# Optimization experiments

Measured on AMD Instinct MI355X. Metric: run time of the kernel, lower is better.

The kernel has to match this reference:

```python
import jax, jax.numpy as jnp
import numpy as np

TOP_K = 2
E = 8      # num_experts
D = 1024   # model dim
F = 2048   # expert hidden dim = int(2*3072/3), already a multiple of 256
B, S = 2, 1024


def setup_inputs() -> dict:
    key = jax.random.key(0)
    ks = jax.random.split(key, 8)
    sc = 0.02
    return {
        "x_bsD": jax.random.normal(ks[0], (B, S, D), dtype=jnp.float32),
        "router_DE": jax.random.normal(ks[1], (D, E), dtype=jnp.float32) * sc,
        "w_in_shared_FD": jax.random.normal(ks[2], (F, D), dtype=jnp.float32) * sc,
        "w_out_shared_DF": jax.random.normal(ks[3], (D, F), dtype=jnp.float32) * sc,
        "w_swiglu_FD": jax.random.normal(ks[4], (F, D), dtype=jnp.float32) * sc,
        "w_in_eDF": jax.random.normal(ks[5], (E, D, F), dtype=jnp.float32) * sc,
        "w_swiglu_eDF": jax.random.normal(ks[6], (E, D, F), dtype=jnp.float32) * sc,
        "w_out_eFD": jax.random.normal(ks[7], (E, F, D), dtype=jnp.float32) * sc,
    }


def reference(x_bsD, router_DE, w_in_shared_FD, w_out_shared_DF, w_swiglu_FD,
              w_in_eDF, w_swiglu_eDF, w_out_eFD):
    b, s, d = x_bsD.shape
    x_aD = x_bsD.reshape(-1, d)                      # [a, D]
    a = x_aD.shape[0]

    # Router (token choice): top-k per token, others masked to -inf
    scores_aE = x_aD @ router_DE                      # [a, E]
    topv_aK, topi_aK = jax.lax.top_k(scores_aE, TOP_K)
    masked_aE = jnp.full_like(scores_aE, -jnp.inf)
    masked_aE = masked_aE.at[jnp.arange(a)[:, None], topi_aK].set(topv_aK)
    # sigmoid(-inf) == 0 -> non-selected (expert, token) pairs contribute nothing
    gates_Ea = jax.nn.sigmoid(masked_aE.astype(jnp.float32)).astype(x_aD.dtype).T  # [E, a]

    # Dispatch: router_indices_EG == arange(a) per expert, so gather == broadcast
    routed_in_EaD = x_aD[None, :, :] * gates_Ea[:, :, None]   # [E, a, D]
    routed_in_EaD = jax.lax.stop_gradient(routed_in_EaD)      # matches .detach()

    # Per-expert bmm SwiGLU
    mid_EaF = jnp.einsum('ead,edf->eaf', routed_in_EaD, w_in_eDF)
    sw_EaF = jnp.einsum('ead,edf->eaf', routed_in_EaD, w_swiglu_eDF)
    h_EaF = jax.nn.silu(mid_EaF) * sw_EaF
    out_EaD = jnp.einsum('eaf,efd->ead', h_EaF, w_out_eFD)

    # Shared expert (computed under torch.no_grad in the original)
    shared_aF = jax.nn.silu(x_aD @ w_in_shared_FD.T) * (x_aD @ w_swiglu_FD.T)
    shared_out_aD = jax.lax.stop_gradient(shared_aF @ w_out_shared_DF.T)

    # Combine: scatter_add with per-expert arange indices == sum over experts
    out_aD = shared_out_aD + jnp.sum(out_EaD, axis=0)
    return out_aD.reshape(b, s, d)
```

## Files before the change

kernel.cpp:

```cpp
#include <hip/hip_runtime.h>
#include <hip/hip_bf16.h>

#define A_TOK 2048
#define DDIM 1024
#define FDIM 2048
#define NEXP 8
#define NE9 9
#define SLOTS_R (2 * A_TOK)
#define SLOTS_T (SLOTS_R + A_TOK)

typedef __attribute__((ext_vector_type(8))) short short8v;
typedef __attribute__((ext_vector_type(4))) float f32x4;

#define BARRIER() asm volatile("s_barrier" ::: "memory")
#define VMCNT(n) asm volatile("s_waitcnt vmcnt(" #n ")" ::: "memory")

__device__ __forceinline__ void lds16(const void* g, void* l) {
  __builtin_amdgcn_global_load_lds((const __attribute__((address_space(1))) void*)g,
                                   (__attribute__((address_space(3))) void*)l, 16, 0, 0);
}

__device__ __forceinline__ float sigmoidf_(float x) { return 1.f / (1.f + __expf(-x)); }

__device__ __forceinline__ void stage_unit(const ushort* gbase, size_t grow0,
                                           int K, int k0, char* lds, int tid) {
  int o = tid * 16;
  int row = o >> 6;
  int g = (o >> 4) & 3;
  int gg = g ^ ((row >> 1) & 3);
  lds16((const char*)(gbase + (grow0 + row) * (size_t)K + k0 + gg * 8), lds + o);
}

__global__ void k_cvt3(const float* __restrict__ s0, const float* __restrict__ s1,
                       const float* __restrict__ s2, __hip_bfloat16* __restrict__ d0,
                       __hip_bfloat16* __restrict__ d1, __hip_bfloat16* __restrict__ d2) {
  const float* in = blockIdx.z == 0 ? s0 : (blockIdx.z == 1 ? s1 : s2);
  __hip_bfloat16* out = blockIdx.z == 0 ? d0 : (blockIdx.z == 1 ? d1 : d2);
  int j = (blockIdx.x * blockDim.x + threadIdx.x) * 4;
  float4 v = *(const float4*)(in + j);
  out[j + 0] = __float2bfloat16(v.x);
  out[j + 1] = __float2bfloat16(v.y);
  out[j + 2] = __float2bfloat16(v.z);
  out[j + 3] = __float2bfloat16(v.w);
}

__global__ void k_transpose(const float* __restrict__ in, __hip_bfloat16* __restrict__ out,
                            int R, int C) {
  __shared__ __hip_bfloat16 tile[64][66];
  size_t zofs = (size_t)blockIdx.z * R * C;
  in += zofs; out += zofs;
  int r0 = blockIdx.y * 64, c0 = blockIdx.x * 64;
  int rr = threadIdx.x >> 6;
  int cc = threadIdx.x & 63;
#pragma unroll
  for (int i = 0; i < 16; i++) {
    int r = i * 4 + rr;
    tile[r][cc] = __float2bfloat16(in[(size_t)(r0 + r) * C + c0 + cc]);
  }
  __syncthreads();
#pragma unroll
  for (int i = 0; i < 16; i++) {
    int c = i * 4 + rr;
    out[(size_t)(c0 + c) * R + r0 + cc] = tile[cc][c];
  }
}

__global__ void k_router(const float* __restrict__ x, const float* __restrict__ rw,
                         __hip_bfloat16* __restrict__ xbf, int* __restrict__ counts,
                         int* __restrict__ top_e, float* __restrict__ top_g) {
  int t = blockIdx.x * 4 + (threadIdx.x >> 6);
  int l = threadIdx.x & 63;
  const float* xr = x + (size_t)t * DDIM;
  float acc[NEXP];
#pragma unroll
  for (int e = 0; e < NEXP; e++) acc[e] = 0.f;
#pragma unroll
  for (int i = 0; i < 16; i++) {
    int d = i * 64 + l;
    float v = xr[d];
    xbf[(size_t)t * DDIM + d] = __float2bfloat16(v);
    const float* rr = rw + (size_t)d * NEXP;
#pragma unroll
    for (int e = 0; e < NEXP; e++) acc[e] += v * rr[e];
  }
#pragma unroll
  for (int e = 0; e < NEXP; e++) {
#pragma unroll
    for (int s = 32; s > 0; s >>= 1) acc[e] += __shfl_xor(acc[e], s);
  }
  if (l == 0) {
    float b1 = -1e30f, b2 = -1e30f;
    int i1 = 0, i2 = 0;
#pragma unroll
    for (int e = 0; e < NEXP; e++) {
      float v = acc[e];
      if (v > b1) { b2 = b1; i2 = i1; b1 = v; i1 = e; }
      else if (v > b2) { b2 = v; i2 = e; }
    }
    atomicAdd(&counts[i1], 1);
    atomicAdd(&counts[i2], 1);
    top_e[t * 2 + 0] = i1; top_e[t * 2 + 1] = i2;
    top_g[t * 2 + 0] = sigmoidf_(b1); top_g[t * 2 + 1] = sigmoidf_(b2);
  }
}

__global__ void k_scan(int* __restrict__ counts, int* __restrict__ offs,
                       int* __restrict__ cursor) {
  if (threadIdx.x == 0 && blockIdx.x == 0) {
    counts[NEXP] = A_TOK;
    int s = 0;
    for (int e = 0; e < NE9; e++) { offs[e] = s; s += counts[e]; cursor[e] = 0; }
  }
}

__global__ void k_dispatch(const float* __restrict__ x, const int* __restrict__ top_e,
                           const float* __restrict__ top_g, const int* __restrict__ offs,
                           int* __restrict__ cursor, int* __restrict__ slot_of,
                           __hip_bfloat16* __restrict__ y) {
  int t = blockIdx.x * 4 + (threadIdx.x >> 6);
  int l = threadIdx.x & 63;
  int e0 = top_e[t * 2 + 0], e1 = top_e[t * 2 + 1];
  float g0 = top_g[t * 2 + 0], g1 = top_g[t * 2 + 1];
  int s0 = 0, s1 = 0;
  if (l == 0) {
    s0 = offs[e0] + atomicAdd(&cursor[e0], 1);
    s1 = offs[e1] + atomicAdd(&cursor[e1], 1);
    slot_of[t * 2 + 0] = s0; slot_of[t * 2 + 1] = s1;
  }
  s0 = __shfl(s0, 0); s1 = __shfl(s1, 0);
  const float* xr = x + (size_t)t * DDIM;
#pragma unroll
  for (int i = 0; i < 16; i++) {
    int d = i * 64 + l;
    float v = xr[d];
    y[(size_t)s0 * DDIM + d] = __float2bfloat16(v * g0);
    y[(size_t)s1 * DDIM + d] = __float2bfloat16(v * g1);
  }
}

__global__ __launch_bounds__(512, 2) void k_mlp1(
    const ushort* __restrict__ Abase, const ushort* __restrict__ B1base,
    const ushort* __restrict__ B2base, ushort* __restrict__ Obase,
    const int* __restrict__ d_cnt, const int* __restrict__ d_off) {
  constexpr int K = DDIM, NT = DDIM / 32;
  constexpr int BUF = 40960;
  __shared__ __align__(16) char smem[3 * BUF];
  int e = blockIdx.z;
  int cnt = d_cnt[e];
  int m0 = blockIdx.y * 128;
  if (m0 >= cnt) return;
  int roff = d_off[e];
  int n0 = blockIdx.x * 256;
  const ushort* B1 = B1base + (size_t)e * FDIM * DDIM;
  const ushort* B2 = B2base + (size_t)e * FDIM * DDIM;
  int tid = threadIdx.x;
  int w = tid >> 6, l = tid & 63;
  int wm = w >> 2, wn = w & 3;
  int lr = l & 15, kg = l >> 4;
  size_t arow0 = (size_t)roff + m0;

  f32x4 acc1[4][4], acc2[4][4];
#pragma unroll
  for (int i = 0; i < 4; i++)
#pragma unroll
    for (int j = 0; j < 4; j++) {
      acc1[i][j] = {0.f, 0.f, 0.f, 0.f};
      acc2[i][j] = {0.f, 0.f, 0.f, 0.f};
    }

  auto frag = [&](const char* base, int row) -> short8v {
    return *(const short8v*)(base + row * 64 + ((kg ^ ((row >> 1) & 3)) << 4));
  };

#pragma unroll
  for (int pt = 0; pt < 2; ++pt) {
    char* bb = smem + pt * BUF;
    int k0 = pt * 32;
    stage_unit(Abase, arow0, K, k0, bb, tid);
    stage_unit(B1, (size_t)n0, K, k0, bb + 8192, tid);
    stage_unit(B1, (size_t)n0 + 128, K, k0, bb + 16384, tid);
    stage_unit(B2, (size_t)n0, K, k0, bb + 24576, tid);
    stage_unit(B2, (size_t)n0 + 128, K, k0, bb + 32768, tid);
  }
  VMCNT(5);
  BARRIER();

  char* b0 = smem;
  char* b1 = smem + BUF;
  char* b2 = smem + 2 * BUF;
  for (int t = 0; t < NT; ++t) {
    bool st = (t + 2) < NT;
    int k2 = (t + 2) * 32;
    short8v af[4], bf[4];
#pragma unroll
    for (int mf = 0; mf < 4; mf++) af[mf] = frag(b0, wm * 64 + mf * 16 + lr);
#pragma unroll
    for (int nf = 0; nf < 4; nf++) bf[nf] = frag(b0 + 8192, wn * 64 + nf * 16 + lr);
    if (st) {
      stage_unit(Abase, arow0, K, k2, b2, tid);
      stage_unit(B1, (size_t)n0, K, k2, b2 + 8192, tid);
    }
    BARRIER();
    __builtin_amdgcn_s_setprio(1);
#pragma unroll
    for (int nf = 0; nf < 4; nf++)
#pragma unroll
      for (int mf = 0; mf < 4; mf++)
        acc1[mf][nf] = __builtin_amdgcn_mfma_f32_16x16x32_bf16(af[mf], bf[nf], acc1[mf][nf], 0, 0, 0);
    __builtin_amdgcn_s_setprio(0);
    BARRIER();
#pragma unroll
    for (int nf = 0; nf < 4; nf++) bf[nf] = frag(b0 + 24576, wn * 64 + nf * 16 + lr);
    if (st) {
      stage_unit(B1, (size_t)n0 + 128, K, k2, b2 + 16384, tid);
      stage_unit(B2, (size_t)n0, K, k2, b2 + 24576, tid);
      stage_unit(B2, (size_t)n0 + 128, K, k2, b2 + 32768, tid);
    }
    BARRIER();
    __builtin_amdgcn_s_setprio(1);
#pragma unroll
    for (int nf = 0; nf < 4; nf++)
#pragma unroll
      for (int mf = 0; mf < 4; mf++)
        acc2[mf][nf] = __builtin_amdgcn_mfma_f32_16x16x32_bf16(af[mf], bf[nf], acc2[mf][nf], 0, 0, 0);
    __builtin_amdgcn_s_setprio(0);
    if (t < NT - 1) {
      if (st) { VMCNT(5); } else { VMCNT(0); }
      BARRIER();
    }
    char* tmp = b0; b0 = b1; b1 = b2; b2 = tmp;
  }

#pragma unroll
  for (int mf = 0; mf < 4; mf++)
#pragma unroll
    for (int nf = 0; nf < 4; nf++)
#pragma unroll
      for (int r = 0; r < 4; r++) {
        int row = m0 + wm * 64 + mf * 16 + kg * 4 + r;
        if (row < cnt) {
          float mid = acc1[mf][nf][r];
          float sw = acc2[mf][nf][r];
          float h = mid * sigmoidf_(mid) * sw;
          int col = n0 + wn * 64 + nf * 16 + lr;
          __hip_bfloat16 hb = __float2bfloat16(h);
          ushort u; __builtin_memcpy(&u, &hb, 2);
          Obase[((size_t)roff + row) * FDIM + col] = u;
        }
      }
}

__global__ __launch_bounds__(512, 4) void k_mlp2(
    const ushort* __restrict__ Abase, const ushort* __restrict__ Bbase,
    float* __restrict__ part, const int* __restrict__ d_cnt, const int* __restrict__ d_off) {
  constexpr int K = FDIM, NT = 1024 / 32;
  constexpr int BUF = 24576;
  __shared__ __align__(16) char smem[3 * BUF];
  int e = blockIdx.z;
  int cnt = d_cnt[e];
  int mt = blockIdx.y >> 1, kz = blockIdx.y & 1;
  int m0 = mt * 128;
  if (m0 >= cnt) return;
  int roff = d_off[e];
  int n0 = blockIdx.x * 256;
  int kbeg = kz * 1024;
  const ushort* B = Bbase + (size_t)e * DDIM * FDIM;
  int tid = threadIdx.x;
  int w = tid >> 6, l = tid & 63;
  int wm = w >> 2, wn = w & 3;
  int lr = l & 15, kg = l >> 4;
  size_t arow0 = (size_t)roff + m0;

  f32x4 acc[4][4];
#pragma unroll
  for (int i = 0; i < 4; i++)
#pragma unroll
    for (int j = 0; j < 4; j++) acc[i][j] = {0.f, 0.f, 0.f, 0.f};

  auto frag = [&](const char* base, int row) -> short8v {
    return *(const short8v*)(base + row * 64 + ((kg ^ ((row >> 1) & 3)) << 4));
  };

#pragma unroll
  for (int pt = 0; pt < 2; ++pt) {
    char* bb = smem + pt * BUF;
    int k0 = kbeg + pt * 32;
    stage_unit(Abase, arow0, K, k0, bb, tid);
    stage_unit(B, (size_t)n0, K, k0, bb + 8192, tid);
    stage_unit(B, (size_t)n0 + 128, K, k0, bb + 16384, tid);
  }
  VMCNT(3);
  BARRIER();

  char* b0 = smem;
  char* b1 = smem + BUF;
  char* b2 = smem + 2 * BUF;
  for (int t = 0; t < NT; ++t) {
    bool st = (t + 2) < NT;
    int k2 = kbeg + (t + 2) * 32;
    short8v af[4], bf[4];
#pragma unroll
    for (int mf = 0; mf < 4; mf++) af[mf] = frag(b0, wm * 64 + mf * 16 + lr);
#pragma unroll
    for (int nf = 0; nf < 4; nf++) bf[nf] = frag(b0 + 8192, wn * 64 + nf * 16 + lr);
    if (st) {
      stage_unit(Abase, arow0, K, k2, b2, tid);
      stage_unit(B, (size_t)n0, K, k2, b2 + 8192, tid);
    }
    BARRIER();
    __builtin_amdgcn_s_setprio(1);
#pragma unroll
    for (int nf = 0; nf < 2; nf++)
#pragma unroll
      for (int mf = 0; mf < 4; mf++)
        acc[mf][nf] = __builtin_amdgcn_mfma_f32_16x16x32_bf16(af[mf], bf[nf], acc[mf][nf], 0, 0, 0);
    __builtin_amdgcn_s_setprio(0);
    BARRIER();
    if (st) stage_unit(B, (size_t)n0 + 128, K, k2, b2 + 16384, tid);
    __builtin_amdgcn_s_setprio(1);
#pragma unroll
    for (int nf = 2; nf < 4; nf++)
#pragma unroll
      for (int mf = 0; mf < 4; mf++)
        acc[mf][nf] = __builtin_amdgcn_mfma_f32_16x16x32_bf16(af[mf], bf[nf], acc[mf][nf], 0, 0, 0);
    __builtin_amdgcn_s_setprio(0);
    if (t < NT - 1) {
      if (st) { VMCNT(3); } else { VMCNT(0); }
      BARRIER();
    }
    char* tmp = b0; b0 = b1; b1 = b2; b2 = tmp;
  }

  float* outp = part + (size_t)kz * SLOTS_T * DDIM;
#pragma unroll
  for (int mf = 0; mf < 4; mf++)
#pragma unroll
    for (int nf = 0; nf < 4; nf++)
#pragma unroll
      for (int r = 0; r < 4; r++) {
        int row = m0 + wm * 64 + mf * 16 + kg * 4 + r;
        if (row < cnt) {
          int col = n0 + wn * 64 + nf * 16 + lr;
          outp[((size_t)roff + row) * DDIM + col] = acc[mf][nf][r];
        }
      }
}

__global__ void k_combine(const float* __restrict__ part, const int* __restrict__ slot_of,
                          float* __restrict__ out) {
  int t = blockIdx.x;
  int d4 = threadIdx.x;
  int s0 = slot_of[t * 2 + 0], s1 = slot_of[t * 2 + 1];
  const float4* p0 = (const float4*)part;
  const float4* p1 = (const float4*)(part + (size_t)SLOTS_T * DDIM);
  size_t rq = DDIM / 4;
  float4 a = p0[(size_t)s0 * rq + d4];
  float4 b = p0[(size_t)s1 * rq + d4];
  float4 c = p0[((size_t)SLOTS_R + t) * rq + d4];
  float4 d = p1[(size_t)s0 * rq + d4];
  float4 e = p1[(size_t)s1 * rq + d4];
  float4 f = p1[((size_t)SLOTS_R + t) * rq + d4];
  float4 o;
  o.x = a.x + b.x + c.x + d.x + e.x + f.x;
  o.y = a.y + b.y + c.y + d.y + e.y + f.y;
  o.z = a.z + b.z + c.z + d.z + e.z + f.z;
  o.w = a.w + b.w + c.w + d.w + e.w + f.w;
  ((float4*)out)[(size_t)t * rq + d4] = o;
}

extern "C" void kernel_launch(void* const* d_in, const int* in_sizes, int n_in,
                              void* d_out, int out_size, void* d_ws, size_t ws_size,
                              hipStream_t stream) {
  (void)in_sizes; (void)n_in; (void)out_size; (void)ws_size;
  const float* x        = (const float*)d_in[0];
  const float* router   = (const float*)d_in[1];
  const float* w_in_sh  = (const float*)d_in[2];
  const float* w_out_sh = (const float*)d_in[3];
  const float* w_sw_sh  = (const float*)d_in[4];
  const float* w_in_e   = (const float*)d_in[5];
  const float* w_sw_e   = (const float*)d_in[6];
  const float* w_out_e  = (const float*)d_in[7];
  float* out = (float*)d_out;

  char* ws = (char*)d_ws;
  size_t off = 0;
  auto alloc = [&](size_t bytes) -> char* {
    char* p = ws + off;
    off += (bytes + 255) & ~(size_t)255;
    return p;
  };
  __hip_bfloat16* wt_in_t  = (__hip_bfloat16*)alloc((size_t)NE9 * FDIM * DDIM * 2);
  __hip_bfloat16* wt_sw_t  = (__hip_bfloat16*)alloc((size_t)NE9 * FDIM * DDIM * 2);
  __hip_bfloat16* wt_out_t = (__hip_bfloat16*)alloc((size_t)NE9 * DDIM * FDIM * 2);
  __hip_bfloat16* y_all    = (__hip_bfloat16*)alloc((size_t)SLOTS_R * DDIM * 2);
  __hip_bfloat16* xbf      = (__hip_bfloat16*)alloc((size_t)A_TOK * DDIM * 2);
  __hip_bfloat16* h        = (__hip_bfloat16*)alloc((size_t)SLOTS_T * FDIM * 2);
  int*   counts  = (int*)alloc(64);
  int*   offs    = (int*)alloc(64);
  int*   cursor  = (int*)alloc(64);
  int*   top_e   = (int*)alloc((size_t)A_TOK * 2 * 4);
  float* top_g   = (float*)alloc((size_t)A_TOK * 2 * 4);
  int*   slot_of = (int*)alloc((size_t)A_TOK * 2 * 4);
  float* slot_part = (float*)wt_in_t;

  hipMemsetAsync(counts, 0, 64, stream);

  k_cvt3<<<dim3((FDIM * DDIM / 4) / 256, 1, 3), 256, 0, stream>>>(
      w_in_sh, w_sw_sh, w_out_sh,
      wt_in_t + (size_t)NEXP * FDIM * DDIM,
      wt_sw_t + (size_t)NEXP * FDIM * DDIM,
      wt_out_t + (size_t)NEXP * DDIM * FDIM);
  k_transpose<<<dim3(FDIM / 64, DDIM / 64, NEXP), 256, 0, stream>>>(w_in_e, wt_in_t, DDIM, FDIM);
  k_transpose<<<dim3(FDIM / 64, DDIM / 64, NEXP), 256, 0, stream>>>(w_sw_e, wt_sw_t, DDIM, FDIM);
  k_transpose<<<dim3(DDIM / 64, FDIM / 64, NEXP), 256, 0, stream>>>(w_out_e, wt_out_t, FDIM, DDIM);

  k_router<<<dim3(A_TOK / 4), 256, 0, stream>>>(x, router, xbf, counts, top_e, top_g);
  k_scan<<<1, 64, 0, stream>>>(counts, offs, cursor);
  k_dispatch<<<dim3(A_TOK / 4), 256, 0, stream>>>(x, top_e, top_g, offs, cursor, slot_of, y_all);

  k_mlp1<<<dim3(FDIM / 256, A_TOK / 128, NE9), 512, 0, stream>>>(
      (const ushort*)y_all, (const ushort*)wt_in_t, (const ushort*)wt_sw_t,
      (ushort*)h, counts, offs);

  k_mlp2<<<dim3(DDIM / 256, (A_TOK / 128) * 2, NE9), 512, 0, stream>>>(
      (const ushort*)h, (const ushort*)wt_out_t, slot_part, counts, offs);

  k_combine<<<dim3(A_TOK), 256, 0, stream>>>(slot_part, slot_of, out);
}
```

Baseline: 307.5 us.

## Interleave gate/up weights into one matrix and shrink GEMM tiles to 128x128

Expert in-projection and SwiGLU weights are transposed into one interleaved matrix, with 32-row blocks alternating, so the first GEMM stages a single B operand. Each 128x128 tile then holds matching mid and swiglu columns for the fused SiLU product. Both GEMMs move from 512-thread 128x256 tiles to 256-thread 128x128 tiles with smaller LDS buffers, giving more resident blocks and more blocks in the grid. The split-K partial results are stored as bf16 instead of fp32, which halves partial-sum traffic into the combine kernel but adds rounding error, and the shared-expert weight conversion is rewritten as a row-wise vectorized kernel.

Measured after the change: 305.0 us. About the same (-0.8%).

```diff
diff --git a/kernel.cpp b/kernel.cpp
--- a/kernel.cpp
+++ b/kernel.cpp
@@ -8,9 +8,11 @@
 #define NE9 9
 #define SLOTS_R (2 * A_TOK)
 #define SLOTS_T (SLOTS_R + A_TOK)
+#define NB1 (2 * FDIM)
 
 typedef __attribute__((ext_vector_type(8))) short short8v;
 typedef __attribute__((ext_vector_type(4))) float f32x4;
+typedef __attribute__((ext_vector_type(4))) ushort ushort4v;
 
 #define BARRIER() asm volatile("s_barrier" ::: "memory")
 #define VMCNT(n) asm volatile("s_waitcnt vmcnt(" #n ")" ::: "memory")
@@ -21,9 +23,16 @@
 }
 
 __device__ __forceinline__ float sigmoidf_(float x) { return 1.f / (1.f + __expf(-x)); }
-
-__device__ __forceinline__ void stage_unit(const ushort* gbase, size_t grow0,
-                                           int K, int k0, char* lds, int tid) {
+__device__ __forceinline__ ushort f2bf(float x) {
+  __hip_bfloat16 b = __float2bfloat16(x);
+  ushort u; __builtin_memcpy(&u, &b, 2); return u;
+}
+__device__ __forceinline__ float bf2f(ushort u) {
+  union { unsigned int i; float f; } x; x.i = (unsigned int)u << 16; return x.f;
+}
+
+__device__ __forceinline__ void stage64(const ushort* gbase, size_t grow0,
+                                        int K, int k0, char* lds, int tid) {
   int o = tid * 16;
   int row = o >> 6;
   int g = (o >> 4) & 3;
@@ -31,37 +40,70 @@
   lds16((const char*)(gbase + (grow0 + row) * (size_t)K + k0 + gg * 8), lds + o);
 }
 
-__global__ void k_cvt3(const float* __restrict__ s0, const float* __restrict__ s1,
-                       const float* __restrict__ s2, __hip_bfloat16* __restrict__ d0,
-                       __hip_bfloat16* __restrict__ d1, __hip_bfloat16* __restrict__ d2) {
-  const float* in = blockIdx.z == 0 ? s0 : (blockIdx.z == 1 ? s1 : s2);
-  __hip_bfloat16* out = blockIdx.z == 0 ? d0 : (blockIdx.z == 1 ? d1 : d2);
-  int j = (blockIdx.x * blockDim.x + threadIdx.x) * 4;
-  float4 v = *(const float4*)(in + j);
-  out[j + 0] = __float2bfloat16(v.x);
-  out[j + 1] = __float2bfloat16(v.y);
-  out[j + 2] = __float2bfloat16(v.z);
-  out[j + 3] = __float2bfloat16(v.w);
-}
-
-__global__ void k_transpose(const float* __restrict__ in, __hip_bfloat16* __restrict__ out,
+__global__ void k_tr12(const float* __restrict__ w_in, const float* __restrict__ w_sw,
+                       ushort* __restrict__ wt12) {
+  int z = blockIdx.z; int e = z & 7; int which = z >> 3;
+  const float* in = (which ? w_sw : w_in) + (size_t)e * DDIM * FDIM;
+  ushort* outb = wt12 + (size_t)e * NB1 * DDIM;
+  __shared__ ushort tile[64][66];
+  int r0 = blockIdx.y * 64, c0 = blockIdx.x * 64;
+  int rr = threadIdx.x >> 6, cc = threadIdx.x & 63;
+#pragma unroll
+  for (int i = 0; i < 16; i++) {
+    int r = i * 4 + rr;
+    tile[r][cc] = f2bf(in[(size_t)(r0 + r) * FDIM + c0 + cc]);
+  }
+  __syncthreads();
+#pragma unroll
+  for (int i = 0; i < 16; i++) {
+    int c = i * 4 + rr;
+    int f = c0 + c;
+    int rp = ((f >> 5) << 6) + (which << 5) + (f & 31);
+    outb[(size_t)rp * DDIM + r0 + cc] = tile[cc][c];
+  }
+}
+
+__global__ void k_transpose(const float* __restrict__ in, ushort* __restrict__ out,
                             int R, int C) {
-  __shared__ __hip_bfloat16 tile[64][66];
-  size_t zofs = (size_t)blockIdx.z * R * C;
-  in += zofs; out += zofs;
+  __shared__ ushort tile[64][66];
+  in += (size_t)blockIdx.z * R * C;
+  out += (size_t)blockIdx.z * R * C;
   int r0 = blockIdx.y * 64, c0 = blockIdx.x * 64;
-  int rr = threadIdx.x >> 6;
-  int cc = threadIdx.x & 63;
+  int rr = threadIdx.x >> 6, cc = threadIdx.x & 63;
 #pragma unroll
   for (int i = 0; i < 16; i++) {
     int r = i * 4 + rr;
-    tile[r][cc] = __float2bfloat16(in[(size_t)(r0 + r) * C + c0 + cc]);
+    tile[r][cc] = f2bf(in[(size_t)(r0 + r) * C + c0 + cc]);
   }
   __syncthreads();
 #pragma unroll
   for (int i = 0; i < 16; i++) {
     int c = i * 4 + rr;
     out[(size_t)(c0 + c) * R + r0 + cc] = tile[cc][c];
+  }
+}
+
+__global__ void k_cvt_sh(const float* __restrict__ w_in_sh, const float* __restrict__ w_sw_sh,
+                         const float* __restrict__ w_out_sh, ushort* __restrict__ wt12_8,
+                         ushort* __restrict__ wtout_8) {
+  int z = blockIdx.y, row = blockIdx.x, tid = threadIdx.x;
+  if (z < 2) {
+    const float* in = (z ? w_sw_sh : w_in_sh) + (size_t)row * DDIM;
+    int rp = ((row >> 5) << 6) + (z << 5) + (row & 31);
+    ushort* outr = wt12_8 + (size_t)rp * DDIM;
+    float4 v = ((const float4*)in)[tid];
+    ushort4v o = {f2bf(v.x), f2bf(v.y), f2bf(v.z), f2bf(v.w)};
+    ((ushort4v*)outr)[tid] = o;
+  } else {
+    if (row >= DDIM) return;
+    const float* in = w_out_sh + (size_t)row * FDIM;
+    ushort* outr = wtout_8 + (size_t)row * FDIM;
+#pragma unroll
+    for (int i = 0; i < 2; i++) {
+      float4 v = ((const float4*)in)[tid + 256 * i];
+      ushort4v o = {f2bf(v.x), f2bf(v.y), f2bf(v.z), f2bf(v.w)};
+      ((ushort4v*)outr)[tid + 256 * i] = o;
+    }
   }
 }
 
@@ -138,35 +180,29 @@
   }
 }
 
-__global__ __launch_bounds__(512, 2) void k_mlp1(
-    const ushort* __restrict__ Abase, const ushort* __restrict__ B1base,
-    const ushort* __restrict__ B2base, ushort* __restrict__ Obase,
-    const int* __restrict__ d_cnt, const int* __restrict__ d_off) {
+__global__ __launch_bounds__(256, 3) void k_mlp1(
+    const ushort* __restrict__ Abase, const ushort* __restrict__ Bbase,
+    ushort* __restrict__ Obase, const int* __restrict__ d_cnt,
+    const int* __restrict__ d_off) {
   constexpr int K = DDIM, NT = DDIM / 32;
-  constexpr int BUF = 40960;
+  constexpr int BUF = 16384;
   __shared__ __align__(16) char smem[3 * BUF];
   int e = blockIdx.z;
   int cnt = d_cnt[e];
   int m0 = blockIdx.y * 128;
   if (m0 >= cnt) return;
   int roff = d_off[e];
-  int n0 = blockIdx.x * 256;
-  const ushort* B1 = B1base + (size_t)e * FDIM * DDIM;
-  const ushort* B2 = B2base + (size_t)e * FDIM * DDIM;
-  int tid = threadIdx.x;
-  int w = tid >> 6, l = tid & 63;
-  int wm = w >> 2, wn = w & 3;
-  int lr = l & 15, kg = l >> 4;
+  int n0 = blockIdx.x * 128;
+  const ushort* B = Bbase + (size_t)e * NB1 * DDIM;
+  int tid = threadIdx.x, w = tid >> 6, l = tid & 63;
+  int wm = w >> 1, wn = w & 1, lr = l & 15, kg = l >> 4;
   size_t arow0 = (size_t)roff + m0;
 
-  f32x4 acc1[4][4], acc2[4][4];
+  f32x4 acc[4][4];
 #pragma unroll
   for (int i = 0; i < 4; i++)
 #pragma unroll
-    for (int j = 0; j < 4; j++) {
-      acc1[i][j] = {0.f, 0.f, 0.f, 0.f};
-      acc2[i][j] = {0.f, 0.f, 0.f, 0.f};
-    }
+    for (int j = 0; j < 4; j++) acc[i][j] = {0.f, 0.f, 0.f, 0.f};
 
   auto frag = [&](const char* base, int row) -> short8v {
     return *(const short8v*)(base + row * 64 + ((kg ^ ((row >> 1) & 3)) << 4));
@@ -176,13 +212,12 @@
   for (int pt = 0; pt < 2; ++pt) {
     char* bb = smem + pt * BUF;
     int k0 = pt * 32;
-    stage_unit(Abase, arow0, K, k0, bb, tid);
-    stage_unit(B1, (size_t)n0, K, k0, bb + 8192, tid);
-    stage_unit(B1, (size_t)n0 + 128, K, k0, bb + 16384, tid);
-    stage_unit(B2, (size_t)n0, K, k0, bb + 24576, tid);
-    stage_unit(B2, (size_t)n0 + 128, K, k0, bb + 32768, tid);
-  }
-  VMCNT(5);
+    stage64(Abase, arow0, K, k0, bb, tid);
+    stage64(Abase, arow0 + 64, K, k0, bb + 4096, tid);
+    stage64(B, (size_t)n0, K, k0, bb + 8192, tid);
+    stage64(B, (size_t)n0 + 64, K, k0, bb + 12288, tid);
+  }
+  VMCNT(4);
   BARRIER();
 
   char* b0 = smem;
@@ -195,66 +230,65 @@
 #pragma unroll
     for (int mf = 0; mf < 4; mf++) af[mf] = frag(b0, wm * 64 + mf * 16 + lr);
 #pragma unroll
-    for (int nf = 0; nf < 4; nf++) bf[nf] = frag(b0 + 8192, wn * 64 + nf * 16 + lr);
+    for (int nf = 0; nf < 2; nf++) bf[nf] = frag(b0 + 8192, wn * 64 + nf * 16 + lr);
     if (st) {
-      stage_unit(Abase, arow0, K, k2, b2, tid);
-      stage_unit(B1, (size_t)n0, K, k2, b2 + 8192, tid);
+      stage64(Abase, arow0, K, k2, b2, tid);
+      stage64(Abase, arow0 + 64, K, k2, b2 + 4096, tid);
     }
     BARRIER();
     __builtin_amdgcn_s_setprio(1);
 #pragma unroll
-    for (int nf = 0; nf < 4; nf++)
+    for (int nf = 0; nf < 2; nf++)
 #pragma unroll
       for (int mf = 0; mf < 4; mf++)
-        acc1[mf][nf] = __builtin_amdgcn_mfma_f32_16x16x32_bf16(af[mf], bf[nf], acc1[mf][nf], 0, 0, 0);
+        acc[mf][nf] = __builtin_amdgcn_mfma_f32_16x16x32_bf16(af[mf], bf[nf], acc[mf][nf], 0, 0, 0);
     __builtin_amdgcn_s_setprio(0);
     BARRIER();
 #pragma unroll
-    for (int nf = 0; nf < 4; nf++) bf[nf] = frag(b0 + 24576, wn * 64 + nf * 16 + lr);
+    for (int nf = 2; nf < 4; nf++) bf[nf] = frag(b0 + 8192, wn * 64 + nf * 16 + lr);
     if (st) {
-      stage_unit(B1, (size_t)n0 + 128, K, k2, b2 + 16384, tid);
-      stage_unit(B2, (size_t)n0, K, k2, b2 + 24576, tid);
-      stage_unit(B2, (size_t)n0 + 128, K, k2, b2 + 32768, tid);
+      stage64(B, (size_t)n0, K, k2, b2 + 8192, tid);
+      stage64(B, (size_t)n0 + 64, K, k2, b2 + 12288, tid);
     }
     BARRIER();
     __builtin_amdgcn_s_setprio(1);
 #pragma unroll
-    for (int nf = 0; nf < 4; nf++)
+    for (int nf = 2; nf < 4; nf++)
 #pragma unroll
       for (int mf = 0; mf < 4; mf++)
-        acc2[mf][nf] = __builtin_amdgcn_mfma_f32_16x16x32_bf16(af[mf], bf[nf], acc2[mf][nf], 0, 0, 0);
+        acc[mf][nf] = __builtin_amdgcn_mfma_f32_16x16x32_bf16(af[mf], bf[nf], acc[mf][nf], 0, 0, 0);
     __builtin_amdgcn_s_setprio(0);
     if (t < NT - 1) {
-      if (st) { VMCNT(5); } else { VMCNT(0); }
+      if (st) { VMCNT(4); } else { VMCNT(0); }
       BARRIER();
     }
     char* tmp = b0; b0 = b1; b1 = b2; b2 = tmp;
   }
 
+  int j = (n0 >> 6) + wn;
 #pragma unroll
   for (int mf = 0; mf < 4; mf++)
 #pragma unroll
-    for (int nf = 0; nf < 4; nf++)
+    for (int nf = 0; nf < 2; nf++)
 #pragma unroll
       for (int r = 0; r < 4; r++) {
         int row = m0 + wm * 64 + mf * 16 + kg * 4 + r;
         if (row < cnt) {
-          float mid = acc1[mf][nf][r];
-          float sw = acc2[mf][nf][r];
-          float h = mid * sigmoidf_(mid) * sw;
-          int col = n0 + wn * 64 + nf * 16 + lr;
-          __hip_bfloat16 hb = __float2bfloat16(h);
-          ushort u; __builtin_memcpy(&u, &hb, 2);
-          Obase[((size_t)roff + row) * FDIM + col] = u;
+          float mid = acc[mf][nf][r];
+          float sw = acc[mf][nf + 2][r];
+          float hv = mid * sigmoidf_(mid) * sw;
+          int col = j * 32 + nf * 16 + lr;
+          Obase[((size_t)roff + row) * FDIM + col] = f2bf(hv);
         }
       }
 }
 
-__global__ __launch_bounds__(512, 4) void k_mlp2(
+__global__ __launch_bounds__(256, 3) void k_mlp2(
     const ushort* __restrict__ Abase, const ushort* __restrict__ Bbase,
-    float* __restrict__ part, const int* __restrict__ d_cnt, const int* __restrict__ d_off) {
+    ushort* __restrict__ part, const int* __restrict__ d_cnt,
+    const int* __restrict__ d_off) {
   constexpr int K = FDIM, NT = 1024 / 32;
-  constexpr int BUF = 24576;
+  constexpr int BUF = 16384;
   __shared__ __align__(16) char smem[3 * BUF];
   int e = blockIdx.z;
   int cnt = d_cnt[e];
@@ -262,13 +296,11 @@
   int m0 = mt * 128;
   if (m0 >= cnt) return;
   int roff = d_off[e];
-  int n0 = blockIdx.x * 256;
+  int n0 = blockIdx.x * 128;
   int kbeg = kz * 1024;
   const ushort* B = Bbase + (size_t)e * DDIM * FDIM;
-  int tid = threadIdx.x;
-  int w = tid >> 6, l = tid & 63;
-  int wm = w >> 2, wn = w & 3;
-  int lr = l & 15, kg = l >> 4;
+  int tid = threadIdx.x, w = tid >> 6, l = tid & 63;
+  int wm = w >> 1, wn = w & 1, lr = l & 15, kg = l >> 4;
   size_t arow0 = (size_t)roff + m0;
 
   f32x4 acc[4][4];
@@ -285,11 +317,12 @@
   for (int pt = 0; pt < 2; ++pt) {
     char* bb = smem + pt * BUF;
     int k0 = kbeg + pt * 32;
-    stage_unit(Abase, arow0, K, k0, bb, tid);
-    stage_unit(B, (size_t)n0, K, k0, bb + 8192, tid);
-    stage_unit(B, (size_t)n0 + 128, K, k0, bb + 16384, tid);
-  }
-  VMCNT(3);
+    stage64(Abase, arow0, K, k0, bb, tid);
+    stage64(Abase, arow0 + 64, K, k0, bb + 4096, tid);
+    stage64(B, (size_t)n0, K, k0, bb + 8192, tid);
+    stage64(B, (size_t)n0 + 64, K, k0, bb + 12288, tid);
+  }
+  VMCNT(4);
   BARRIER();
 
   char* b0 = smem;
@@ -302,10 +335,10 @@
 #pragma unroll
     for (int mf = 0; mf < 4; mf++) af[mf] = frag(b0, wm * 64 + mf * 16 + lr);
 #pragma unroll
-    for (int nf = 0; nf < 4; nf++) bf[nf] = frag(b0 + 8192, wn * 64 + nf * 16 + lr);
+    for (int nf = 0; nf < 2; nf++) bf[nf] = frag(b0 + 8192, wn * 64 + nf * 16 + lr);
     if (st) {
-      stage_unit(Abase, arow0, K, k2, b2, tid);
-      stage_unit(B, (size_t)n0, K, k2, b2 + 8192, tid);
+      stage64(Abase, arow0, K, k2, b2, tid);
+      stage64(Abase, arow0 + 64, K, k2, b2 + 4096, tid);
     }
     BARRIER();
     __builtin_amdgcn_s_setprio(1);
@@ -316,7 +349,13 @@
         acc[mf][nf] = __builtin_amdgcn_mfma_f32_16x16x32_bf16(af[mf], bf[nf], acc[mf][nf], 0, 0, 0);
     __builtin_amdgcn_s_setprio(0);
     BARRIER();
-    if (st) stage_unit(B, (size_t)n0 + 128, K, k2, b2 + 16384, tid);
+#pragma unroll
+    for (int nf = 2; nf < 4; nf++) bf[nf] = frag(b0 + 8192, wn * 64 + nf * 16 + lr);
+    if (st) {
+      stage64(B, (size_t)n0, K, k2, b2 + 8192, tid);
+      stage64(B, (size_t)n0 + 64, K, k2, b2 + 12288, tid);
+    }
+    BARRIER();
     __builtin_amdgcn_s_setprio(1);
 #pragma unroll
     for (int nf = 2; nf < 4; nf++)
@@ -325,13 +364,13 @@
         acc[mf][nf] = __builtin_amdgcn_mfma_f32_16x16x32_bf16(af[mf], bf[nf], acc[mf][nf], 0, 0, 0);
     __builtin_amdgcn_s_setprio(0);
     if (t < NT - 1) {
-      if (st) { VMCNT(3); } else { VMCNT(0); }
+      if (st) { VMCNT(4); } else { VMCNT(0); }
       BARRIER();
     }
     char* tmp = b0; b0 = b1; b1 = b2; b2 = tmp;
   }
 
-  float* outp = part + (size_t)kz * SLOTS_T * DDIM;
+  ushort* outp = part + (size_t)kz * SLOTS_T * DDIM;
 #pragma unroll
   for (int mf = 0; mf < 4; mf++)
 #pragma unroll
@@ -341,31 +380,30 @@
         int row = m0 + wm * 64 + mf * 16 + kg * 4 + r;
         if (row < cnt) {
           int col = n0 + wn * 64 + nf * 16 + lr;
-          outp[((size_t)roff + row) * DDIM + col] = acc[mf][nf][r];
+          outp[((size_t)roff + row) * DDIM + col] = f2bf(acc[mf][nf][r]);
         }
       }
 }
 
-__global__ void k_combine(const float* __restrict__ part, const int* __restrict__ slot_of,
+__global__ void k_combine(const ushort* __restrict__ part, const int* __restrict__ slot_of,
                           float* __restrict__ out) {
-  int t = blockIdx.x;
-  int d4 = threadIdx.x;
-  int s0 = slot_of[t * 2 + 0], s1 = slot_of[t * 2 + 1];
-  const float4* p0 = (const float4*)part;
-  const float4* p1 = (const float4*)(part + (size_t)SLOTS_T * DDIM);
-  size_t rq = DDIM / 4;
-  float4 a = p0[(size_t)s0 * rq + d4];
-  float4 b = p0[(size_t)s1 * rq + d4];
-  float4 c = p0[((size_t)SLOTS_R + t) * rq + d4];
-  float4 d = p1[(size_t)s0 * rq + d4];
-  float4 e = p1[(size_t)s1 * rq + d4];
-  float4 f = p1[((size_t)SLOTS_R + t) * rq + d4];
-  float4 o;
-  o.x = a.x + b.x + c.x + d.x + e.x + f.x;
-  o.y = a.y + b.y + c.y + d.y + e.y + f.y;
-  o.z = a.z + b.z + c.z + d.z + e.z + f.z;
-  o.w = a.w + b.w + c.w + d.w + e.w + f.w;
-  ((float4*)out)[(size_t)t * rq + d4] = o;
+  int t = blockIdx.x, q = threadIdx.x;
+  int rows[3];
+  rows[0] = slot_of[t * 2 + 0];
+  rows[1] = slot_of[t * 2 + 1];
+  rows[2] = SLOTS_R + t;
+  size_t P = (size_t)SLOTS_T * DDIM;
+  float o[4] = {0.f, 0.f, 0.f, 0.f};
+#pragma unroll
+  for (int kz = 0; kz < 2; kz++)
+#pragma unroll
+    for (int i = 0; i < 3; i++) {
+      ushort4v v = *(const ushort4v*)(part + kz * P + (size_t)rows[i] * DDIM + q * 4);
+#pragma unroll
+      for (int j = 0; j < 4; j++) o[j] += bf2f(v[j]);
+    }
+  float4 ov = {o[0], o[1], o[2], o[3]};
+  ((float4*)out)[(size_t)t * (DDIM / 4) + q] = ov;
 }
 
 extern "C" void kernel_launch(void* const* d_in, const int* in_sizes, int n_in,
@@ -389,41 +427,37 @@
     off += (bytes + 255) & ~(size_t)255;
     return p;
   };
-  __hip_bfloat16* wt_in_t  = (__hip_bfloat16*)alloc((size_t)NE9 * FDIM * DDIM * 2);
-  __hip_bfloat16* wt_sw_t  = (__hip_bfloat16*)alloc((size_t)NE9 * FDIM * DDIM * 2);
-  __hip_bfloat16* wt_out_t = (__hip_bfloat16*)alloc((size_t)NE9 * DDIM * FDIM * 2);
-  __hip_bfloat16* y_all    = (__hip_bfloat16*)alloc((size_t)SLOTS_R * DDIM * 2);
-  __hip_bfloat16* xbf      = (__hip_bfloat16*)alloc((size_t)A_TOK * DDIM * 2);
-  __hip_bfloat16* h        = (__hip_bfloat16*)alloc((size_t)SLOTS_T * FDIM * 2);
+  ushort* wt12     = (ushort*)alloc((size_t)NE9 * NB1 * DDIM * 2);
+  ushort* wt_out_t = (ushort*)alloc((size_t)NE9 * DDIM * FDIM * 2);
+  __hip_bfloat16* y_all = (__hip_bfloat16*)alloc((size_t)SLOTS_R * DDIM * 2);
+  __hip_bfloat16* xbf   = (__hip_bfloat16*)alloc((size_t)A_TOK * DDIM * 2);
+  ushort* h        = (ushort*)alloc((size_t)SLOTS_T * FDIM * 2);
   int*   counts  = (int*)alloc(64);
   int*   offs    = (int*)alloc(64);
   int*   cursor  = (int*)alloc(64);
   int*   top_e   = (int*)alloc((size_t)A_TOK * 2 * 4);
   float* top_g   = (float*)alloc((size_t)A_TOK * 2 * 4);
   int*   slot_of = (int*)alloc((size_t)A_TOK * 2 * 4);
-  float* slot_part = (float*)wt_in_t;
+  (void)alloc(1 << 20);
+  ushort* part = wt12;
 
   hipMemsetAsync(counts, 0, 64, stream);
 
-  k_cvt3<<<dim3((FDIM * DDIM / 4) / 256, 1, 3), 256, 0, stream>>>(
+  k_tr12<<<dim3(FDIM / 64, DDIM / 64, 16), 256, 0, stream>>>(w_in_e, w_sw_e, wt12);
+  k_transpose<<<dim3(DDIM / 64, FDIM / 64, NEXP), 256, 0, stream>>>(w_out_e, wt_out_t, FDIM, DDIM);
+  k_cvt_sh<<<dim3(FDIM, 3), 256, 0, stream>>>(
       w_in_sh, w_sw_sh, w_out_sh,
-      wt_in_t + (size_t)NEXP * FDIM * DDIM,
-      wt_sw_t + (size_t)NEXP * FDIM * DDIM,
-      wt_out_t + (size_t)NEXP * DDIM * FDIM);
-  k_transpose<<<dim3(FDIM / 64, DDIM / 64, NEXP), 256, 0, stream>>>(w_in_e, wt_in_t, DDIM, FDIM);
-  k_transpose<<<dim3(FDIM / 64, DDIM / 64, NEXP), 256, 0, stream>>>(w_sw_e, wt_sw_t, DDIM, FDIM);
-  k_transpose<<<dim3(DDIM / 64, FDIM / 64, NEXP), 256, 0, stream>>>(w_out_e, wt_out_t, FDIM, DDIM);
+      wt12 + (size_t)NEXP * NB1 * DDIM, wt_out_t + (size_t)NEXP * DDIM * FDIM);
 
   k_router<<<dim3(A_TOK / 4), 256, 0, stream>>>(x, router, xbf, counts, top_e, top_g);
   k_scan<<<1, 64, 0, stream>>>(counts, offs, cursor);
   k_dispatch<<<dim3(A_TOK / 4), 256, 0, stream>>>(x, top_e, top_g, offs, cursor, slot_of, y_all);
 
-  k_mlp1<<<dim3(FDIM / 256, A_TOK / 128, NE9), 512, 0, stream>>>(
-      (const ushort*)y_all, (const ushort*)wt_in_t, (const ushort*)wt_sw_t,
-      (ushort*)h, counts, offs);
-
-  k_mlp2<<<dim3(DDIM / 256, (A_TOK / 128) * 2, NE9), 512, 0, stream>>>(
-      (const ushort*)h, (const ushort*)wt_out_t, slot_part, counts, offs);
-
-  k_combine<<<dim3(A_TOK), 256, 0, stream>>>(slot_part, slot_of, out);
-}
+  k_mlp1<<<dim3(NB1 / 128, A_TOK / 128, NE9), 256, 0, stream>>>(
+      (const ushort*)y_all, wt12, h, counts, offs);
+
+  k_mlp2<<<dim3(DDIM / 128, (A_TOK / 128) * 2, NE9), 256, 0, stream>>>(
+      h, wt_out_t, part, counts, offs);
+
+  k_combine<<<dim3(A_TOK), 256, 0, stream>>>(part, slot_of, out);
+}
```
